# Kernel tuning notes

Measured on AMD Instinct MI355X. Metric: run time of the kernel, lower is better.

## Reference

```python
import jax, jax.numpy as jnp
import numpy as np

NMS_PRE_MAXSIZE = 4096
NMS_POST_MAXSIZE = 512
NMS_THRESH = 0.7


def setup_inputs() -> dict:
    key = jax.random.key(0)
    k1, k2, k3, k4, k5 = jax.random.split(key, 5)
    B, N, C = 4, 32768, 3
    # realistic 3D boxes: (x, y, z, dx, dy, dz, heading)
    xy = jax.random.uniform(k1, (B, N, 2), dtype=jnp.float32) * 70.0
    z = jax.random.uniform(k2, (B, N, 1), dtype=jnp.float32) * 4.0 - 2.0
    sizes = jax.random.uniform(k3, (B, N, 3), dtype=jnp.float32) * 3.0 + 1.0
    heading = jax.random.uniform(k4, (B, N, 1), dtype=jnp.float32) * 6.2832 - 3.1416
    batch_box_preds = jnp.concatenate([xy, z, sizes, heading], axis=-1)  # (B,N,7)
    batch_cls_preds = jax.random.uniform(k5, (B, N, C), dtype=jnp.float32)  # (B,N,3)
    return {"batch_box_preds": batch_box_preds, "batch_cls_preds": batch_cls_preds}


def _nms_single(boxes, scores, labels):
    # boxes (N,7), scores (N,), labels (N,) int32
    top_s, idx = jax.lax.top_k(scores, NMS_PRE_MAXSIZE)   # sort desc, keep pre-maxsize
    b = boxes[idx]                                        # (PRE,7)
    l = labels[idx]
    # BEV axis-aligned IoU (reference surrogate for the rotated-BEV CUDA IoU kernel)
    x, y, dx, dy = b[:, 0], b[:, 1], b[:, 3], b[:, 4]
    x1, x2 = x - 0.5 * dx, x + 0.5 * dx
    y1, y2 = y - 0.5 * dy, y + 0.5 * dy
    area = dx * dy
    ix = jnp.maximum(0.0, jnp.minimum(x2[:, None], x2[None, :]) - jnp.maximum(x1[:, None], x1[None, :]))
    iy = jnp.maximum(0.0, jnp.minimum(y2[:, None], y2[None, :]) - jnp.maximum(y1[:, None], y1[None, :]))
    inter = ix * iy
    iou = jax.lax.stop_gradient(inter / (area[:, None] + area[None, :] - inter + 1e-6))

    ar = jnp.arange(NMS_PRE_MAXSIZE)

    def body(i, keep):
        sup = (iou[i] > NMS_THRESH) & (ar > i) & keep[i]
        return keep & ~sup

    keep = jax.lax.fori_loop(0, NMS_PRE_MAXSIZE, body, jnp.ones(NMS_PRE_MAXSIZE, bool))

    # pack first NMS_POST_MAXSIZE kept boxes into fixed-size zero-padded outputs
    rank = jnp.cumsum(keep) - 1
    valid = keep & (rank < NMS_POST_MAXSIZE)
    pos = jnp.where(valid, rank, NMS_POST_MAXSIZE)  # invalid -> scratch row
    rois = jnp.zeros((NMS_POST_MAXSIZE + 1, 7), b.dtype).at[pos].set(b)[:NMS_POST_MAXSIZE]
    sc = jnp.zeros((NMS_POST_MAXSIZE + 1,), top_s.dtype).at[pos].set(top_s)[:NMS_POST_MAXSIZE]
    lb = jnp.zeros((NMS_POST_MAXSIZE + 1,), jnp.int32).at[pos].set(l)[:NMS_POST_MAXSIZE]
    return rois, sc, lb


def reference(batch_box_preds, batch_cls_preds):
    # per-box max score / argmax class (torch.max(cls_preds, dim=1) per sample)
    roi_scores_all = jnp.max(batch_cls_preds, axis=-1)                 # (B,N)
    roi_labels_all = jnp.argmax(batch_cls_preds, axis=-1).astype(jnp.int32)
    rois, roi_scores, roi_labels = jax.vmap(_nms_single)(batch_box_preds, roi_scores_all, roi_labels_all)
    return rois, roi_scores, roi_labels + 1  # labels shifted by +1 as in proposal_layer
```

## Files before the change

kernel.cpp:

```cpp
#include <hip/hip_runtime.h>
#include <stdint.h>

#define BB 4
#define NN 32768
#define PRE 4096
#define POST 512
#define NMS_TH 0.7f
#define MIDCAP 8192

typedef unsigned long long u64;
typedef unsigned int u32;

__device__ __forceinline__ u32 orderable(float f) {
  u32 u = __float_as_uint(f);
  return (u & 0x80000000u) ? ~u : (u | 0x80000000u);
}
__device__ __forceinline__ float unorderable(u32 o) {
  u32 u = (o & 0x80000000u) ? (o & 0x7fffffffu) : ~o;
  return __uint_as_float(u);
}
__device__ __forceinline__ u32 bucket_of(float s) {
  u32 v = (u32)(s * 2147483648.0f);
  u32 bk = v >> 20;
  return bk > 2047u ? 2047u : bk;
}

__global__ void zero_kernel(u32* __restrict__ hist, u32* __restrict__ cnt_mid) {
  int t = blockIdx.x * 256 + threadIdx.x;
  if (t < BB * 2048) hist[t] = 0;
  if (t < BB) cnt_mid[t] = 0;
}

__global__ __launch_bounds__(256) void score_hist_kernel(const float* __restrict__ cls,
                                                         int* __restrict__ labels,
                                                         u64* __restrict__ keys,
                                                         u32* __restrict__ hist) {
  __shared__ u32 lh[2048];
  for (int t = threadIdx.x; t < 2048; t += 256) lh[t] = 0;
  __syncthreads();
  int g = blockIdx.x * 256 + threadIdx.x;
  const float* c = cls + (size_t)g * 3;
  float s = c[0]; int l = 0;
  float c1 = c[1], c2 = c[2];
  if (c1 > s) { s = c1; l = 1; }
  if (c2 > s) { s = c2; l = 2; }
  int n = g & (NN - 1);
  keys[g] = ((u64)orderable(s) << 32) | (u32)(~(u32)n);
  labels[g] = l;
  atomicAdd(&lh[bucket_of(s)], 1u);
  __syncthreads();
  int b = blockIdx.x >> 7;
  for (int t = threadIdx.x; t < 2048; t += 256) {
    u32 v = lh[t];
    if (v) atomicAdd(&hist[b * 2048 + t], v);
  }
}

__global__ __launch_bounds__(256) void select_kernel(const u32* __restrict__ hist,
                                                     u32* __restrict__ selinfo,
                                                     u32* __restrict__ sfxBuf,
                                                     u32* __restrict__ cursor) {
  __shared__ u32 sfx[2048];
  int b = blockIdx.x;
  for (int t = threadIdx.x; t < 2048; t += 256) sfx[t] = hist[b * 2048 + t];
  __syncthreads();
  for (int d = 1; d < 2048; d <<= 1) {
    u32 v[8];
#pragma unroll
    for (int i = 0; i < 8; ++i) {
      int t = threadIdx.x + i * 256;
      v[i] = (t + d < 2048) ? sfx[t + d] : 0;
    }
    __syncthreads();
#pragma unroll
    for (int i = 0; i < 8; ++i) sfx[threadIdx.x + i * 256] += v[i];
    __syncthreads();
  }
  for (int t = threadIdx.x; t < 2048; t += 256) {
    u32 above = (t + 1 < 2048) ? sfx[t + 1] : 0;
    sfxBuf[b * 2048 + t] = sfx[t];
    cursor[b * 2048 + t] = above;
    if (above < PRE && sfx[t] >= PRE) { selinfo[b * 2] = (u32)t; selinfo[b * 2 + 1] = above; }
  }
}

__global__ __launch_bounds__(256) void compact_kernel(const u64* __restrict__ keys,
                                                      const u32* __restrict__ selinfo,
                                                      u32* __restrict__ cursor,
                                                      u64* __restrict__ sel, u64* __restrict__ mid,
                                                      u32* __restrict__ cnt_mid) {
  int g = blockIdx.x * 256 + threadIdx.x;
  int b = g >> 15;
  u64 key = keys[g];
  u32 bk = bucket_of(unorderable((u32)(key >> 32)));
  u32 T = selinfo[b * 2];
  if (bk > T) {
    u32 p = atomicAdd(&cursor[b * 2048 + bk], 1u);
    sel[((size_t)b << 12) + p] = key;
  } else if (bk == T) {
    u32 p = atomicAdd(&cnt_mid[b], 1u);
    if (p < MIDCAP) mid[(size_t)b * MIDCAP + p] = key;
  }
}

__global__ __launch_bounds__(64) void bsort_kernel(u64* __restrict__ sel, u64* __restrict__ mid,
                                                   const u32* __restrict__ sfxBuf,
                                                   const u32* __restrict__ selinfo,
                                                   const u32* __restrict__ cnt_mid) {
  int t = blockIdx.x & 2047;
  int b = blockIdx.x >> 11;
  int lane = threadIdx.x;
  u32 T = selinfo[b * 2];
  u64* selB = sel + ((size_t)b << 12);
  if ((u32)t == T) {
    u32 C1 = selinfo[b * 2 + 1];
    int need = PRE - (int)C1;
    int M = (int)cnt_mid[b]; if (M > MIDCAP) M = MIDCAP;
    u64* midB = mid + (size_t)b * MIDCAP;
    for (int r = 0; r < need; ++r) {
      u64 best = 0; int bi = -1;
      for (int q = lane; q < M; q += 64) {
        u64 v = midB[q];
        if (v > best) { best = v; bi = q; }
      }
#pragma unroll
      for (int d = 32; d > 0; d >>= 1) {
        u64 ob = __shfl_xor(best, d, 64);
        int oi = __shfl_xor(bi, d, 64);
        if (ob > best) { best = ob; bi = oi; }
      }
      if (lane == 0) selB[C1 + r] = best;
      if (bi >= 0 && lane == (bi & 63)) midB[bi] = 0;
    }
    return;
  }
  if ((u32)t < T) return;
  u32 start = (t < 2047) ? sfxBuf[b * 2048 + t + 1] : 0u;
  u32 end = sfxBuf[b * 2048 + t];
  int n = (int)(end - start);
  if (n <= 1) return;
  if (n <= 64) {
    u64 v = (lane < n) ? selB[start + lane] : 0ULL;
#pragma unroll
    for (int k = 2; k <= 64; k <<= 1) {
#pragma unroll
      for (int j = k >> 1; j > 0; j >>= 1) {
        u64 o = __shfl_xor(v, j, 64);
        bool up = ((lane & k) == 0);
        bool first = ((lane & j) == 0);
        u64 mx = v > o ? v : o, mn = v > o ? o : v;
        v = (first == up) ? mx : mn;
      }
    }
    if (lane < n) selB[start + lane] = v;
  } else {
    for (int r = 0; r < n - 1; ++r) {
      u64 best = 0; int bi = -1;
      for (int q = r + lane; q < n; q += 64) {
        u64 v = selB[start + q];
        if (v > best) { best = v; bi = q; }
      }
#pragma unroll
      for (int d = 32; d > 0; d >>= 1) {
        u64 ob = __shfl_xor(best, d, 64);
        int oi = __shfl_xor(bi, d, 64);
        if (ob > best) { best = ob; bi = oi; }
      }
      if (lane == 0) {
        u64 tmp = selB[start + r];
        selB[start + r] = best;
        selB[start + bi] = tmp;
      }
    }
  }
}

__global__ void gather_kernel(const u64* __restrict__ keys, const float* __restrict__ boxes,
                              const int* __restrict__ labels,
                              float* __restrict__ topBox, float4* __restrict__ P,
                              float* __restrict__ AR,
                              float* __restrict__ topS, int* __restrict__ topL) {
  int g = blockIdx.x * blockDim.x + threadIdx.x;
  if (g >= BB * PRE) return;
  int b = g >> 12;
  u64 key = keys[g];
  u32 n = ~(u32)key;
  size_t src = (size_t)b * NN + n;
  const float* bx = boxes + src * 7;
  float x = bx[0], y = bx[1], dx = bx[3], dy = bx[4];
  float* tb = topBox + (size_t)g * 7;
#pragma unroll
  for (int c = 0; c < 7; ++c) tb[c] = bx[c];
  float4 p;
  p.x = x - 0.5f * dx; p.z = x + 0.5f * dx;
  p.y = y - 0.5f * dy; p.w = y + 0.5f * dy;
  P[g] = p;
  AR[g] = dx * dy;
  topS[g] = unorderable((u32)(key >> 32));
  topL[g] = labels[src];
}

__global__ __launch_bounds__(64) void mask_kernel(const float4* __restrict__ P,
                                                  const float* __restrict__ AR,
                                                  u64* __restrict__ maskT,
                                                  u64* __restrict__ diag) {
  int b = blockIdx.y;
  int ti = blockIdx.x;
  int lane = threadIdx.x;
  int u = 2079 - ti;
  int m = (int)((sqrtf(8.0f * (float)u + 1.0f) - 1.0f) * 0.5f);
  while ((m + 1) * (m + 2) / 2 <= u) ++m;
  while (m * (m + 1) / 2 > u) --m;
  int rb = 63 - m;
  int w = rb + (u - m * (m + 1) / 2);
  int base = b << 12;
  int row = (rb << 6) + lane;
  float4 rp = P[base + row];
  float rar = AR[base + row];
  const float4* __restrict__ Pcol = P + base + (w << 6);
  const float* __restrict__ ARcol = AR + base + (w << 6);
  u64 bits = 0;
#pragma unroll
  for (int k = 0; k < 64; ++k) {
    float4 cb = Pcol[k];
    float ca = ARcol[k];
    float ix = fminf(rp.z, cb.z) - fmaxf(rp.x, cb.x); ix = fmaxf(0.0f, ix);
    float iy = fminf(rp.w, cb.w) - fmaxf(rp.y, cb.y); iy = fmaxf(0.0f, iy);
    float inter = ix * iy;
    float denom = ((rar + ca) - inter) + 1e-6f;
    float t = 0.7f * denom;
    bool sup;
    bool marginal = fabsf(inter - t) <= 2e-5f * t;
    if (__any(marginal)) sup = (inter / denom) > NMS_TH;
    else sup = inter > t;
    bits |= ((u64)(sup ? 1u : 0u)) << k;
  }
  maskT[((size_t)(b * 64 + w)) * PRE + row] = bits;
  if (w == rb) diag[base + row] = bits;
}

__global__ __launch_bounds__(64) void scan_kernel(const u64* __restrict__ maskT,
                                                  const u64* __restrict__ diag,
                                                  int* __restrict__ keepIdx,
                                                  int* __restrict__ keepCount) {
  __shared__ u64 kwLDS[64];
  int b = blockIdx.x;
  int lane = threadIdx.x;
  const u64* m = maskT + (size_t)b * 64 * PRE;
  const u64* dg = diag + (size_t)b * PRE;
  kwLDS[lane] = 0;
  __syncthreads();
  u64 r = 0;
  int nk = 0;
  for (int g = 0; g < PRE / 64; ++g) {
    u64 d_l = dg[g * 64 + lane];
    const ulonglong2* mp = (const ulonglong2*)(m + (size_t)lane * PRE + (g << 6));
    ulonglong2 rv[32];
#pragma unroll
    for (int q = 0; q < 32; ++q) rv[q] = mp[q];
    u64 sup_word = __shfl(r, g, 64);
    u64 keep_word = 0;
#pragma unroll
    for (int s = 0; s < 8; ++s) {
      u64 dk[8];
#pragma unroll
      for (int t = 0; t < 8; ++t) dk[t] = __shfl(d_l, s * 8 + t, 64);
#pragma unroll
      for (int t = 0; t < 8; ++t) {
        int k = s * 8 + t;
        u64 bit = (sup_word >> k) & 1ULL;
        keep_word |= (bit ^ 1ULL) << k;
        u64 mk = dk[t] & ~((2ULL << k) - 1ULL);
        sup_word |= mk & (bit - 1ULL);
      }
    }
    u64 acc = 0;
#pragma unroll
    for (int q = 0; q < 32; ++q) {
      acc |= ((keep_word >> (2 * q)) & 1ULL) ? rv[q].x : 0ULL;
      acc |= ((keep_word >> (2 * q + 1)) & 1ULL) ? rv[q].y : 0ULL;
    }
    r |= acc;
    if (lane == 0) kwLDS[g] = keep_word;
    nk += __popcll(keep_word);
    if (nk >= POST) break;
  }
  __syncthreads();
  u64 kw = kwLDS[lane];
  int cnt = __popcll(kw);
  int pfx = cnt;
#pragma unroll
  for (int d = 1; d < 64; d <<= 1) {
    int up = __shfl_up(pfx, d, 64);
    if (lane >= d) pfx += up;
  }
  int total = __shfl(pfx, 63, 64);
  int pos = pfx - cnt;
  while (kw) {
    int t = __ffsll((long long)kw) - 1;
    kw &= kw - 1;
    if (pos < POST) keepIdx[b * POST + pos] = lane * 64 + t;
    ++pos;
  }
  if (lane == 0) keepCount[b] = total < POST ? total : POST;
}

__global__ void output_kernel(const int* __restrict__ keepIdx, const int* __restrict__ keepCount,
                              const float* __restrict__ topBox, const float* __restrict__ topS,
                              const int* __restrict__ topL, float* __restrict__ out) {
  int g = blockIdx.x * blockDim.x + threadIdx.x;
  if (g >= BB * POST) return;
  int b = g >> 9, s = g & (POST - 1);
  float* outR = out;
  float* outS = out + BB * POST * 7;
  float* outL = outS + BB * POST;
  int cnt = keepCount[b];
  if (s < cnt) {
    int i = keepIdx[g];
    const float* tb = topBox + ((size_t)(b << 12) + i) * 7;
#pragma unroll
    for (int c = 0; c < 7; ++c) outR[(size_t)g * 7 + c] = tb[c];
    outS[g] = topS[(b << 12) + i];
    outL[g] = (float)(topL[(b << 12) + i] + 1);
  } else {
#pragma unroll
    for (int c = 0; c < 7; ++c) outR[(size_t)g * 7 + c] = 0.0f;
    outS[g] = 0.0f;
    outL[g] = 1.0f;
  }
}

extern "C" void kernel_launch(void* const* d_in, const int* in_sizes, int n_in,
                              void* d_out, int out_size, void* d_ws, size_t ws_size,
                              hipStream_t stream) {
  const float* boxes = (const float*)d_in[0];
  const float* cls   = (const float*)d_in[1];
  float* out = (float*)d_out;

  char* p = (char*)d_ws;
  auto take = [&](size_t bytes) { char* r = p; p += (bytes + 255) & ~(size_t)255; return (void*)r; };
  u64*   keys    = (u64*)  take((size_t)BB * NN * 8);
  int*   labels  = (int*)  take((size_t)BB * NN * 4);
  u32*   hist    = (u32*)  take((size_t)BB * 2048 * 4);
  u32*   selinfo = (u32*)  take((size_t)BB * 2 * 4);
  u32*   sfxBuf  = (u32*)  take((size_t)BB * 2048 * 4);
  u32*   cursor  = (u32*)  take((size_t)BB * 2048 * 4);
  u32*   cnt_mid = (u32*)  take((size_t)BB * 4);
  u64*   sel     = (u64*)  take((size_t)BB * PRE * 8);
  u64*   mid     = (u64*)  take((size_t)BB * MIDCAP * 8);
  float* topBox  = (float*)take((size_t)BB * PRE * 7 * 4);
  float4* Pb     = (float4*)take((size_t)BB * PRE * 16);
  float* AR      = (float*)take((size_t)BB * PRE * 4);
  float* topS    = (float*)take((size_t)BB * PRE * 4);
  int*   topL    = (int*)  take((size_t)BB * PRE * 4);
  u64*   maskT   = (u64*)  take((size_t)BB * 64 * PRE * 8);
  u64*   diagBuf = (u64*)  take((size_t)BB * PRE * 8);
  int*   keepIdx = (int*)  take((size_t)BB * POST * 4);
  int*   keepCnt = (int*)  take((size_t)BB * 4);

  zero_kernel<<<32, 256, 0, stream>>>(hist, cnt_mid);
  score_hist_kernel<<<BB * NN / 256, 256, 0, stream>>>(cls, labels, keys, hist);
  select_kernel<<<BB, 256, 0, stream>>>(hist, selinfo, sfxBuf, cursor);
  compact_kernel<<<BB * NN / 256, 256, 0, stream>>>(keys, selinfo, cursor, sel, mid, cnt_mid);
  bsort_kernel<<<BB * 2048, 64, 0, stream>>>(sel, mid, sfxBuf, selinfo, cnt_mid);
  gather_kernel<<<(BB * PRE + 255) / 256, 256, 0, stream>>>(sel, boxes, labels,
                                                            topBox, Pb, AR, topS, topL);
  mask_kernel<<<dim3(2080, BB), 64, 0, stream>>>(Pb, AR, maskT, diagBuf);
  scan_kernel<<<BB, 64, 0, stream>>>(maskT, diagBuf, keepIdx, keepCnt);
  output_kernel<<<(BB * POST + 255) / 256, 256, 0, stream>>>(keepIdx, keepCnt, topBox, topS, topL, out);
}
```

Measured before the change: 103.9 us.

## Split NMS mask into two phases and skip second when enough boxes kept

Result: no change. 104.2 us (+0.3%).

```diff
diff --git a/kernel.cpp b/kernel.cpp
--- a/kernel.cpp
+++ b/kernel.cpp
@@ -7,6 +7,7 @@
 #define POST 512
 #define NMS_TH 0.7f
 #define MIDCAP 8192
+#define P1G 16
 
 typedef unsigned long long u64;
 typedef unsigned int u32;
@@ -200,19 +201,11 @@
   topL[g] = labels[src];
 }
 
-__global__ __launch_bounds__(64) void mask_kernel(const float4* __restrict__ P,
-                                                  const float* __restrict__ AR,
-                                                  u64* __restrict__ maskT,
-                                                  u64* __restrict__ diag) {
-  int b = blockIdx.y;
-  int ti = blockIdx.x;
-  int lane = threadIdx.x;
-  int u = 2079 - ti;
-  int m = (int)((sqrtf(8.0f * (float)u + 1.0f) - 1.0f) * 0.5f);
-  while ((m + 1) * (m + 2) / 2 <= u) ++m;
-  while (m * (m + 1) / 2 > u) --m;
-  int rb = 63 - m;
-  int w = rb + (u - m * (m + 1) / 2);
+__device__ __forceinline__ void mask_tile(int b, int rb, int w, int lane,
+                                          const float4* __restrict__ P,
+                                          const float* __restrict__ AR,
+                                          u64* __restrict__ maskT,
+                                          u64* __restrict__ diag) {
   int base = b << 12;
   int row = (rb << 6) + lane;
   float4 rp = P[base + row];
@@ -220,7 +213,8 @@
   const float4* __restrict__ Pcol = P + base + (w << 6);
   const float* __restrict__ ARcol = AR + base + (w << 6);
   u64 bits = 0;
-#pragma unroll
+  float margMin = 1.0f;
+#pragma unroll 8
   for (int k = 0; k < 64; ++k) {
     float4 cb = Pcol[k];
     float ca = ARcol[k];
@@ -229,30 +223,81 @@
     float inter = ix * iy;
     float denom = ((rar + ca) - inter) + 1e-6f;
     float t = 0.7f * denom;
-    bool sup;
-    bool marginal = fabsf(inter - t) <= 2e-5f * t;
-    if (__any(marginal)) sup = (inter / denom) > NMS_TH;
-    else sup = inter > t;
-    bits |= ((u64)(sup ? 1u : 0u)) << k;
+    bits |= ((u64)(inter > t ? 1u : 0u)) << k;
+    margMin = fminf(margMin, fabsf(inter - t) - 2e-5f * t);
+  }
+  if (__any(margMin <= 0.0f)) {
+    bits = 0;
+    for (int k = 0; k < 64; ++k) {
+      float4 cb = Pcol[k];
+      float ca = ARcol[k];
+      float ix = fminf(rp.z, cb.z) - fmaxf(rp.x, cb.x); ix = fmaxf(0.0f, ix);
+      float iy = fminf(rp.w, cb.w) - fmaxf(rp.y, cb.y); iy = fmaxf(0.0f, iy);
+      float inter = ix * iy;
+      float denom = ((rar + ca) - inter) + 1e-6f;
+      bits |= ((u64)(((inter / denom) > NMS_TH) ? 1u : 0u)) << k;
+    }
   }
   maskT[((size_t)(b * 64 + w)) * PRE + row] = bits;
   if (w == rb) diag[base + row] = bits;
 }
 
+__global__ __launch_bounds__(256) void mask1_kernel(const float4* __restrict__ P,
+                                                    const float* __restrict__ AR,
+                                                    u64* __restrict__ maskT,
+                                                    u64* __restrict__ diag) {
+  int b = blockIdx.y;
+  int ti = blockIdx.x * 4 + (threadIdx.x >> 6);
+  int lane = threadIdx.x & 63;
+  int rb = 0;
+  while (rb < P1G - 1 && (64 * (rb + 1) - ((rb + 1) * rb) / 2) <= ti) ++rb;
+  int w = rb + (ti - (64 * rb - (rb * (rb - 1)) / 2));
+  mask_tile(b, rb, w, lane, P, AR, maskT, diag);
+}
+
+__global__ __launch_bounds__(256) void mask2_kernel(const float4* __restrict__ P,
+                                                    const float* __restrict__ AR,
+                                                    u64* __restrict__ maskT,
+                                                    u64* __restrict__ diag,
+                                                    const u32* __restrict__ doneFlag) {
+  int b = blockIdx.y;
+  if (doneFlag[b]) return;
+  int ti = blockIdx.x * 4 + (threadIdx.x >> 6);
+  int lane = threadIdx.x & 63;
+  int rr = 0;
+  while (rr < 47 && (48 * (rr + 1) - ((rr + 1) * rr) / 2) <= ti) ++rr;
+  int rb = rr + P1G;
+  int w = rb + (ti - (48 * rr - (rr * (rr - 1)) / 2));
+  mask_tile(b, rb, w, lane, P, AR, maskT, diag);
+}
+
 __global__ __launch_bounds__(64) void scan_kernel(const u64* __restrict__ maskT,
                                                   const u64* __restrict__ diag,
-                                                  int* __restrict__ keepIdx,
-                                                  int* __restrict__ keepCount) {
+                                                  const float* __restrict__ topBox,
+                                                  const float* __restrict__ topS,
+                                                  const int* __restrict__ topL,
+                                                  float* __restrict__ out,
+                                                  u64* __restrict__ rState,
+                                                  u64* __restrict__ kwState,
+                                                  u32* __restrict__ nkState,
+                                                  u32* __restrict__ doneFlag,
+                                                  int phase) {
   __shared__ u64 kwLDS[64];
   int b = blockIdx.x;
   int lane = threadIdx.x;
+  if (phase == 1 && doneFlag[b]) return;
   const u64* m = maskT + (size_t)b * 64 * PRE;
   const u64* dg = diag + (size_t)b * PRE;
-  kwLDS[lane] = 0;
+  u64 r; int nk, gs, ge;
+  if (phase == 0) {
+    kwLDS[lane] = 0; r = 0; nk = 0; gs = 0; ge = P1G;
+  } else {
+    kwLDS[lane] = (lane < P1G) ? kwState[b * 64 + lane] : 0;
+    r = rState[b * 64 + lane]; nk = nkState[b]; gs = P1G; ge = 64;
+  }
   __syncthreads();
-  u64 r = 0;
-  int nk = 0;
-  for (int g = 0; g < PRE / 64; ++g) {
+  bool done = false;
+  for (int g = gs; g < ge; ++g) {
     u64 d_l = dg[g * 64 + lane];
     const ulonglong2* mp = (const ulonglong2*)(m + (size_t)lane * PRE + (g << 6));
     ulonglong2 rv[32];
@@ -283,9 +328,16 @@
     r |= acc;
     if (lane == 0) kwLDS[g] = keep_word;
     nk += __popcll(keep_word);
-    if (nk >= POST) break;
+    if (nk >= POST) { done = true; break; }
   }
   __syncthreads();
+  if (phase == 0 && !done) {
+    rState[b * 64 + lane] = r;
+    if (lane < P1G) kwState[b * 64 + lane] = kwLDS[lane];
+    if (lane == 0) { nkState[b] = nk; doneFlag[b] = 0; }
+    return;
+  }
+  if (phase == 0 && lane == 0) doneFlag[b] = 1;
   u64 kw = kwLDS[lane];
   int cnt = __popcll(kw);
   int pfx = cnt;
@@ -296,33 +348,26 @@
   }
   int total = __shfl(pfx, 63, 64);
   int pos = pfx - cnt;
+  float* outR = out;
+  float* outS = out + BB * POST * 7;
+  float* outL = outS + BB * POST;
   while (kw) {
     int t = __ffsll((long long)kw) - 1;
     kw &= kw - 1;
-    if (pos < POST) keepIdx[b * POST + pos] = lane * 64 + t;
+    if (pos < POST) {
+      int i = (lane << 6) + t;
+      int g = (b << 9) + pos;
+      const float* tb = topBox + ((size_t)(b << 12) + i) * 7;
+#pragma unroll
+      for (int c = 0; c < 7; ++c) outR[(size_t)g * 7 + c] = tb[c];
+      outS[g] = topS[(b << 12) + i];
+      outL[g] = (float)(topL[(b << 12) + i] + 1);
+    }
     ++pos;
   }
-  if (lane == 0) keepCount[b] = total < POST ? total : POST;
-}
-
-__global__ void output_kernel(const int* __restrict__ keepIdx, const int* __restrict__ keepCount,
-                              const float* __restrict__ topBox, const float* __restrict__ topS,
-                              const int* __restrict__ topL, float* __restrict__ out) {
-  int g = blockIdx.x * blockDim.x + threadIdx.x;
-  if (g >= BB * POST) return;
-  int b = g >> 9, s = g & (POST - 1);
-  float* outR = out;
-  float* outS = out + BB * POST * 7;
-  float* outL = outS + BB * POST;
-  int cnt = keepCount[b];
-  if (s < cnt) {
-    int i = keepIdx[g];
-    const float* tb = topBox + ((size_t)(b << 12) + i) * 7;
-#pragma unroll
-    for (int c = 0; c < 7; ++c) outR[(size_t)g * 7 + c] = tb[c];
-    outS[g] = topS[(b << 12) + i];
-    outL[g] = (float)(topL[(b << 12) + i] + 1);
-  } else {
+  int fin = total < POST ? total : POST;
+  for (int s = fin + lane; s < POST; s += 64) {
+    int g = (b << 9) + s;
 #pragma unroll
     for (int c = 0; c < 7; ++c) outR[(size_t)g * 7 + c] = 0.0f;
     outS[g] = 0.0f;
@@ -355,8 +400,10 @@
   int*   topL    = (int*)  take((size_t)BB * PRE * 4);
   u64*   maskT   = (u64*)  take((size_t)BB * 64 * PRE * 8);
   u64*   diagBuf = (u64*)  take((size_t)BB * PRE * 8);
-  int*   keepIdx = (int*)  take((size_t)BB * POST * 4);
-  int*   keepCnt = (int*)  take((size_t)BB * 4);
+  u64*   rState  = (u64*)  take((size_t)BB * 64 * 8);
+  u64*   kwState = (u64*)  take((size_t)BB * 64 * 8);
+  u32*   nkState = (u32*)  take((size_t)BB * 4);
+  u32*   doneFlg = (u32*)  take((size_t)BB * 4);
 
   zero_kernel<<<32, 256, 0, stream>>>(hist, cnt_mid);
   score_hist_kernel<<<BB * NN / 256, 256, 0, stream>>>(cls, labels, keys, hist);
@@ -365,7 +412,10 @@
   bsort_kernel<<<BB * 2048, 64, 0, stream>>>(sel, mid, sfxBuf, selinfo, cnt_mid);
   gather_kernel<<<(BB * PRE + 255) / 256, 256, 0, stream>>>(sel, boxes, labels,
                                                             topBox, Pb, AR, topS, topL);
-  mask_kernel<<<dim3(2080, BB), 64, 0, stream>>>(Pb, AR, maskT, diagBuf);
-  scan_kernel<<<BB, 64, 0, stream>>>(maskT, diagBuf, keepIdx, keepCnt);
-  output_kernel<<<(BB * POST + 255) / 256, 256, 0, stream>>>(keepIdx, keepCnt, topBox, topS, topL, out);
-}
+  mask1_kernel<<<dim3(226, BB), 256, 0, stream>>>(Pb, AR, maskT, diagBuf);
+  scan_kernel<<<BB, 64, 0, stream>>>(maskT, diagBuf, topBox, topS, topL, out,
+                                     rState, kwState, nkState, doneFlg, 0);
+  mask2_kernel<<<dim3(294, BB), 256, 0, stream>>>(Pb, AR, maskT, diagBuf, doneFlg);
+  scan_kernel<<<BB, 64, 0, stream>>>(maskT, diagBuf, topBox, topS, topL, out,
+                                     rState, kwState, nkState, doneFlg, 1);
+}
```
